# Optimization experiments

Measured on AMD Instinct MI355X. Metric: run time of the kernel, lower is better.

The kernel has to match this reference:

```python
import jax, jax.numpy as jnp
import numpy as np

N, E, DIN, H, C, ED = 50000, 500000, 264, 4, 32, 16
HID = H * C   # 128
OUT = 128
NEG_SLOPE = 0.2
LN_EPS = 1e-5


def _ln(x, g, b):
    mu = jnp.mean(x, axis=-1, keepdims=True)
    var = jnp.mean((x - mu) ** 2, axis=-1, keepdims=True)
    return (x - mu) * jax.lax.rsqrt(var + LN_EPS) * g + b


def _segment_softmax(scores, seg, num_segments):
    # scores: (E, H), seg: (E,) destination node ids
    m = jax.ops.segment_max(scores, seg, num_segments=num_segments)
    m = jnp.where(jnp.isfinite(m), m, 0.0)
    ex = jnp.exp(scores - m[seg])
    s = jax.ops.segment_sum(ex, seg, num_segments=num_segments)
    return ex / (s[seg] + 1e-16)


def _gatv2(x, src, dst, edge_attr, Wl, bl, Wr, br, We, att, bias):
    # GATv2Conv (PyG semantics): lin_l -> source, lin_r -> target, lin_edge (no bias)
    n = x.shape[0]
    xl = (x @ Wl + bl).reshape(n, H, C)          # source transform
    xr = (x @ Wr + br).reshape(n, H, C)          # target transform
    ee = (edge_attr @ We).reshape(-1, H, C)      # (E, H, C)
    m = xl[src] + xr[dst] + ee                   # per-edge pre-activation
    g = jnp.where(m > 0, m, NEG_SLOPE * m)       # leaky_relu(0.2)
    score = jnp.einsum('ehc,hc->eh', g, att)     # (E, H)
    alpha = _segment_softmax(score, dst, n)      # softmax over in-edges of each dst
    msg = xl[src] * alpha[..., None]             # (E, H, C)
    out = jax.ops.segment_sum(msg, dst, num_segments=n)
    return out.reshape(n, HID) + bias


def setup_inputs() -> dict:
    key = jax.random.key(0)
    ks = jax.random.split(key, 16)
    r = lambda k, s: jax.random.normal(k, s, dtype=jnp.float32) * 0.05
    return {
        'x': jax.random.normal(ks[0], (N, DIN), jnp.float32),
        'edge_attr': jax.random.normal(ks[1], (E, ED), jnp.float32),
        'Wl1': r(ks[2], (DIN, HID)), 'bl1': jnp.zeros((HID,), jnp.float32),
        'Wr1': r(ks[3], (DIN, HID)), 'br1': jnp.zeros((HID,), jnp.float32),
        'We1': r(ks[4], (ED, HID)), 'att1': r(ks[5], (H, C)), 'bias1': jnp.zeros((HID,), jnp.float32),
        'Wl2': r(ks[6], (HID, HID)), 'bl2': jnp.zeros((HID,), jnp.float32),
        'Wr2': r(ks[7], (HID, HID)), 'br2': jnp.zeros((HID,), jnp.float32),
        'We2': r(ks[8], (ED, HID)), 'att2': r(ks[9], (H, C)), 'bias2': jnp.zeros((HID,), jnp.float32),
        'Wres': r(ks[10], (DIN, HID)), 'bres': jnp.zeros((HID,), jnp.float32),
        'Wout': r(ks[11], (HID, OUT)), 'bout': jnp.zeros((OUT,), jnp.float32),
        'g1': jnp.ones((HID,), jnp.float32), 'bn1': jnp.zeros((HID,), jnp.float32),
        'g2': jnp.ones((HID,), jnp.float32), 'bn2': jnp.zeros((HID,), jnp.float32),
        'go': jnp.ones((OUT,), jnp.float32), 'bo': jnp.zeros((OUT,), jnp.float32),
        'edge_index': jax.random.randint(ks[12], (2, E), 0, N, dtype=jnp.int32),
    }


def reference(x, edge_attr, Wl1, bl1, Wr1, br1, We1, att1, bias1,
              Wl2, bl2, Wr2, br2, We2, att2, bias2,
              Wres, bres, Wout, bout, g1, bn1, g2, bn2, go, bo, edge_index):
    src, dst = edge_index[0], edge_index[1]
    residual = x @ Wres + bres
    h = _gatv2(x, src, dst, edge_attr, Wl1, bl1, Wr1, br1, We1, att1, bias1)
    h = jax.nn.elu(h)
    h = _ln(h + residual, g1, bn1)
    residual = h
    h = _gatv2(h, src, dst, edge_attr, Wl2, bl2, Wr2, br2, We2, att2, bias2)
    h = jax.nn.elu(h)
    h = _ln(h + residual, g2, bn2)
    context = _ln(h @ Wout + bout, go, bo)
    return context
```

## Files before the change

### kernel.cpp

```cpp
#include <hip/hip_runtime.h>
#include <hip/hip_bf16.h>
#include <math.h>
#include <stdint.h>

#define NN 50000
#define NE 500000
#define DIN 264
#define KP1 288
#define HID 128
#define EDIM 16

typedef __attribute__((ext_vector_type(8))) short short8;
typedef __attribute__((ext_vector_type(4))) float f32x4;

__device__ __forceinline__ short f2bf(float v) {
    union { float f; unsigned u; } x; x.f = v;
    unsigned r = x.u + 0x7fff + ((x.u >> 16) & 1);
    return (short)(r >> 16);
}
__device__ __forceinline__ float bf2f(short v) {
    union { float f; unsigned u; } x;
    x.u = ((unsigned)(unsigned short)v) << 16;
    return x.f;
}

__device__ __forceinline__ void gload_lds16(const void* g, void* l) {
    __builtin_amdgcn_global_load_lds(
        (const __attribute__((address_space(1))) unsigned int*)g,
        (__attribute__((address_space(3))) unsigned int*)l, 16, 0, 0);
}

__global__ void k_count(const int* __restrict__ dst, int* __restrict__ cnt) {
    int e = blockIdx.x * blockDim.x + threadIdx.x;
    if (e < NE) atomicAdd(&cnt[dst[e]], 1);
}

__global__ __launch_bounds__(256) void k_scan1(const int* __restrict__ cnt,
                                               int* __restrict__ off, int* __restrict__ bsum) {
    __shared__ int buf[256];
    int b = blockIdx.x, t = threadIdx.x;
    int i = b * 256 + t;
    int v = (i < NN) ? cnt[i] : 0;
    buf[t] = v; __syncthreads();
    for (int s = 1; s < 256; s <<= 1) {
        int u = (t >= s) ? buf[t - s] : 0; __syncthreads();
        buf[t] += u; __syncthreads();
    }
    if (i < NN) off[i + 1] = buf[t];
    if (t == 255) bsum[b] = buf[255];
}

__global__ void k_scan2(int* __restrict__ bsum, int nb) {
    __shared__ int buf[256];
    int t = threadIdx.x;
    int o = (t < nb) ? bsum[t] : 0;
    buf[t] = o; __syncthreads();
    for (int s = 1; s < 256; s <<= 1) {
        int u = (t >= s) ? buf[t - s] : 0; __syncthreads();
        buf[t] += u; __syncthreads();
    }
    if (t < nb) bsum[t] = buf[t] - o;
}

__global__ void k_scan3c(int* __restrict__ off, const int* __restrict__ bsum,
                         int* __restrict__ cur) {
    int j = blockIdx.x * 256 + threadIdx.x;
    if (j > NN) return;
    int v = (j == 0) ? 0 : off[j] + bsum[(j - 1) >> 8];
    off[j] = v;
    if (j < NN) cur[j] = v;
}

__global__ void k_scatter(const int* __restrict__ src, const int* __restrict__ dst,
                          int* __restrict__ cur, int2* __restrict__ csr_se) {
    int e = blockIdx.x * blockDim.x + threadIdx.x;
    if (e < NE) {
        int d = dst[e];
        int p = atomicAdd(&cur[d], 1);
        csr_se[p] = make_int2(src[e], e);
    }
}

__global__ void k_cvt_x(const float* __restrict__ x, short* __restrict__ xb) {
    int idx = blockIdx.x * 256 + threadIdx.x;
    if (idx >= NN * KP1) return;
    int i = idx / KP1, k = idx - i * KP1;
    xb[idx] = (k < DIN) ? f2bf(x[(size_t)i * DIN + k]) : (short)0;
}

__global__ void k_prep_w(const float* __restrict__ Wl1, const float* __restrict__ Wr1,
                         const float* __restrict__ Wres, const float* __restrict__ Wl2,
                         const float* __restrict__ Wr2, const float* __restrict__ Wout,
                         const float* __restrict__ bl1, const float* __restrict__ br1,
                         const float* __restrict__ bres, const float* __restrict__ bl2,
                         const float* __restrict__ br2,
                         short* __restrict__ Wt1, short* __restrict__ Wt2,
                         short* __restrict__ Wt3, float* __restrict__ bcat1,
                         float* __restrict__ bcat2) {
    int idx = blockIdx.x * 256 + threadIdx.x;
    if (idx < 384 * KP1) {
        int n = idx / KP1, k = idx - n * KP1;
        float v = 0.f;
        if (k < DIN) {
            const float* W = (n < 128) ? Wl1 : ((n < 256) ? Wr1 : Wres);
            v = W[(size_t)k * 128 + (n & 127)];
        }
        Wt1[idx] = f2bf(v);
        return;
    }
    idx -= 384 * KP1;
    if (idx < 256 * 128) {
        int n = idx >> 7, k = idx & 127;
        const float* W = (n < 128) ? Wl2 : Wr2;
        Wt2[idx] = f2bf(W[(size_t)k * 128 + (n & 127)]);
        return;
    }
    idx -= 256 * 128;
    if (idx < 128 * 128) {
        int n = idx >> 7, k = idx & 127;
        Wt3[idx] = f2bf(Wout[(size_t)k * 128 + n]);
        return;
    }
    idx -= 128 * 128;
    if (idx < 384) {
        bcat1[idx] = (idx < 128) ? bl1[idx] : ((idx < 256) ? br1[idx - 128] : bres[idx - 256]);
        return;
    }
    idx -= 384;
    if (idx < 256)
        bcat2[idx] = (idx < 128) ? bl2[idx] : br2[idx - 128];
}

template <bool BF16OUT>
__global__ __launch_bounds__(256) void k_mfma_gemm(const short* __restrict__ A,
                                                   const short* __restrict__ Bt,
                                                   const float* __restrict__ bias,
                                                   float* __restrict__ Cf,
                                                   short* __restrict__ Cb,
                                                   int M, int Kpad, int NS) {
    __shared__ short As[128 * 32];
    __shared__ short Bs[128 * 32];
    int t = threadIdx.x;
    int lane = t & 63, wid = t >> 6;
    int wm = (wid & 1) * 64, wn = (wid >> 1) * 64;
    int cl = lane & 15, quad = lane >> 4;
    int row0 = blockIdx.x * 128;
    int col0 = blockIdx.y * 128;

    f32x4 acc[4][4];
#pragma unroll
    for (int i = 0; i < 4; ++i)
#pragma unroll
        for (int j = 0; j < 4; ++j) acc[i][j] = (f32x4)0.f;

    for (int k0 = 0; k0 < Kpad; k0 += 32) {
#pragma unroll
        for (int r = 0; r < 2; ++r) {
            int c = t + r * 256;
            int m = c >> 2;
            int row = row0 + m; if (row >= M) row = M - 1;
            const char* ga = (const char*)A + ((size_t)row * Kpad + k0) * 2 + (c & 3) * 16;
            gload_lds16(ga, (char*)As + c * 16);
            int n = col0 + m;
            const char* gb = (const char*)Bt + ((size_t)n * Kpad + k0) * 2 + (c & 3) * 16;
            gload_lds16(gb, (char*)Bs + c * 16);
        }
        __syncthreads();

        short8 a[4], b[4];
#pragma unroll
        for (int mi = 0; mi < 4; ++mi)
            a[mi] = *(const short8*)&As[(wm + mi * 16 + cl) * 32 + quad * 8];
#pragma unroll
        for (int ni = 0; ni < 4; ++ni)
            b[ni] = *(const short8*)&Bs[(wn + ni * 16 + cl) * 32 + quad * 8];
#pragma unroll
        for (int mi = 0; mi < 4; ++mi)
#pragma unroll
            for (int ni = 0; ni < 4; ++ni)
                acc[mi][ni] = __builtin_amdgcn_mfma_f32_16x16x32_bf16(a[mi], b[ni], acc[mi][ni], 0, 0, 0);
        __syncthreads();
    }

#pragma unroll
    for (int mi = 0; mi < 4; ++mi)
#pragma unroll
        for (int ni = 0; ni < 4; ++ni) {
            int col = col0 + wn + ni * 16 + cl;
            float bv = bias[col];
#pragma unroll
            for (int r = 0; r < 4; ++r) {
                int row = row0 + wm + mi * 16 + quad * 4 + r;
                if (row < M) {
                    float v = acc[mi][ni][r] + bv;
                    if (BF16OUT) Cb[(size_t)row * NS + col] = f2bf(v);
                    else         Cf[(size_t)row * NS + col] = v;
                }
            }
        }
}

__device__ __forceinline__ float block_sum128(float v, volatile float* red) {
#pragma unroll
    for (int o = 32; o > 0; o >>= 1) v += __shfl_down(v, o, 64);
    int w = threadIdx.x >> 6;
    __syncthreads();
    if ((threadIdx.x & 63) == 0) red[w] = v;
    __syncthreads();
    return red[0] + red[1];
}

template <int STRIDE, int NPB>
__global__ __launch_bounds__(128) void k_fused_agg(const int* __restrict__ off,
                                                   const int2* __restrict__ csr_se,
                                                   const short* __restrict__ C,
                                                   const float* __restrict__ ea,
                                                   const float* __restrict__ We,
                                                   const float* __restrict__ att,
                                                   const short* __restrict__ resid, int rstride,
                                                   const float* __restrict__ bias,
                                                   const float* __restrict__ gamma,
                                                   const float* __restrict__ beta,
                                                   short* __restrict__ outb) {
    __shared__ float red[2];
    int t = threadIdx.x;

    float wreg[EDIM];
#pragma unroll
    for (int k = 0; k < EDIM; ++k) wreg[k] = We[k * 128 + t];
    float att_t = att[t], bias_t = bias[t], gamma_t = gamma[t], beta_t = beta[t];

    for (int n = 0; n < NPB; ++n) {
        int i = blockIdx.x * NPB + n;
        int b0 = off[i], b1 = off[i + 1];
        float xr_t = bf2f(C[(size_t)i * STRIDE + 128 + t]);

        float l_run = 0.f, acc = 0.f;
        int pos = b0;
        for (; pos + 2 <= b1; pos += 2) {
            int2 seA = csr_se[pos];
            int2 seB = csr_se[pos + 1];
            const float4* eaA = (const float4*)(ea + (size_t)seA.y * EDIM);
            const float4* eaB = (const float4*)(ea + (size_t)seB.y * EDIM);
            float4 A0 = eaA[0], A1 = eaA[1], A2 = eaA[2], A3 = eaA[3];
            float4 B0 = eaB[0], B1 = eaB[1], B2 = eaB[2], B3 = eaB[3];
            float xlA = bf2f(C[(size_t)seA.x * STRIDE + t]);
            float xlB = bf2f(C[(size_t)seB.x * STRIDE + t]);
            float eA = A0.x * wreg[0];
            eA = fmaf(A0.y, wreg[1], eA);  eA = fmaf(A0.z, wreg[2], eA);
            eA = fmaf(A0.w, wreg[3], eA);  eA = fmaf(A1.x, wreg[4], eA);
            eA = fmaf(A1.y, wreg[5], eA);  eA = fmaf(A1.z, wreg[6], eA);
            eA = fmaf(A1.w, wreg[7], eA);  eA = fmaf(A2.x, wreg[8], eA);
            eA = fmaf(A2.y, wreg[9], eA);  eA = fmaf(A2.z, wreg[10], eA);
            eA = fmaf(A2.w, wreg[11], eA); eA = fmaf(A3.x, wreg[12], eA);
            eA = fmaf(A3.y, wreg[13], eA); eA = fmaf(A3.z, wreg[14], eA);
            eA = fmaf(A3.w, wreg[15], eA);
            float mA = xlA + xr_t + eA;
            float pA = fmaxf(mA, 0.2f * mA) * att_t;
            float eB = B0.x * wreg[0];
            eB = fmaf(B0.y, wreg[1], eB);  eB = fmaf(B0.z, wreg[2], eB);
            eB = fmaf(B0.w, wreg[3], eB);  eB = fmaf(B1.x, wreg[4], eB);
            eB = fmaf(B1.y, wreg[5], eB);  eB = fmaf(B1.z, wreg[6], eB);
            eB = fmaf(B1.w, wreg[7], eB);  eB = fmaf(B2.x, wreg[8], eB);
            eB = fmaf(B2.y, wreg[9], eB);  eB = fmaf(B2.z, wreg[10], eB);
            eB = fmaf(B2.w, wreg[11], eB); eB = fmaf(B3.x, wreg[12], eB);
            eB = fmaf(B3.y, wreg[13], eB); eB = fmaf(B3.z, wreg[14], eB);
            eB = fmaf(B3.w, wreg[15], eB);
            float mB = xlB + xr_t + eB;
            float pB = fmaxf(mB, 0.2f * mB) * att_t;
            pA += __shfl_xor(pA, 1, 64);  pB += __shfl_xor(pB, 1, 64);
            pA += __shfl_xor(pA, 2, 64);  pB += __shfl_xor(pB, 2, 64);
            pA += __shfl_xor(pA, 4, 64);  pB += __shfl_xor(pB, 4, 64);
            pA += __shfl_xor(pA, 8, 64);  pB += __shfl_xor(pB, 8, 64);
            pA += __shfl_xor(pA, 16, 64); pB += __shfl_xor(pB, 16, 64);
            float peA = __expf(pA), peB = __expf(pB);
            l_run += peA + peB;
            acc = fmaf(peA, xlA, acc);
            acc = fmaf(peB, xlB, acc);
        }
        if (pos < b1) {
            int2 se = csr_se[pos];
            const float4* ea4 = (const float4*)(ea + (size_t)se.y * EDIM);
            float4 A0 = ea4[0], A1 = ea4[1], A2 = ea4[2], A3 = ea4[3];
            float xlv = bf2f(C[(size_t)se.x * STRIDE + t]);
            float ee = A0.x * wreg[0];
            ee = fmaf(A0.y, wreg[1], ee);  ee = fmaf(A0.z, wreg[2], ee);
            ee = fmaf(A0.w, wreg[3], ee);  ee = fmaf(A1.x, wreg[4], ee);
            ee = fmaf(A1.y, wreg[5], ee);  ee = fmaf(A1.z, wreg[6], ee);
            ee = fmaf(A1.w, wreg[7], ee);  ee = fmaf(A2.x, wreg[8], ee);
            ee = fmaf(A2.y, wreg[9], ee);  ee = fmaf(A2.z, wreg[10], ee);
            ee = fmaf(A2.w, wreg[11], ee); ee = fmaf(A3.x, wreg[12], ee);
            ee = fmaf(A3.y, wreg[13], ee); ee = fmaf(A3.z, wreg[14], ee);
            ee = fmaf(A3.w, wreg[15], ee);
            float m = xlv + xr_t + ee;
            float p = fmaxf(m, 0.2f * m) * att_t;
            p += __shfl_xor(p, 1, 64);
            p += __shfl_xor(p, 2, 64);
            p += __shfl_xor(p, 4, 64);
            p += __shfl_xor(p, 8, 64);
            p += __shfl_xor(p, 16, 64);
            float pe = __expf(p);
            l_run += pe;
            acc = fmaf(pe, xlv, acc);
        }

        float o = acc / (l_run + 1e-16f) + bias_t;
        o = o > 0.f ? o : (__expf(o) - 1.f);
        float v = o + bf2f(resid[(size_t)i * rstride + t]);
        float mean = block_sum128(v, red) * (1.f / 128.f);
        float d = v - mean;
        float var = block_sum128(d * d, red) * (1.f / 128.f);
        float r = d * rsqrtf(var + 1e-5f) * gamma_t + beta_t;
        outb[(size_t)i * 128 + t] = f2bf(r);
    }
}

__global__ __launch_bounds__(128) void k_ln(const float* __restrict__ in,
                                            const float* __restrict__ gamma,
                                            const float* __restrict__ beta,
                                            float* __restrict__ out) {
    __shared__ float red[2];
    int i = blockIdx.x, t = threadIdx.x;
    float v = in[(size_t)i * 128 + t];
    float mean = block_sum128(v, red) * (1.f / 128.f);
    float d = v - mean;
    float var = block_sum128(d * d, red) * (1.f / 128.f);
    out[(size_t)i * 128 + t] = d * rsqrtf(var + 1e-5f) * gamma[t] + beta[t];
}

extern "C" void kernel_launch(void* const* d_in, const int* in_sizes, int n_in,
                              void* d_out, int out_size, void* d_ws, size_t ws_size,
                              hipStream_t stream) {
    (void)in_sizes; (void)n_in; (void)out_size; (void)ws_size;
    const float* x     = (const float*)d_in[0];
    const float* ea    = (const float*)d_in[1];
    const float* Wl1   = (const float*)d_in[2];
    const float* bl1   = (const float*)d_in[3];
    const float* Wr1   = (const float*)d_in[4];
    const float* br1   = (const float*)d_in[5];
    const float* We1   = (const float*)d_in[6];
    const float* att1  = (const float*)d_in[7];
    const float* bias1 = (const float*)d_in[8];
    const float* Wl2   = (const float*)d_in[9];
    const float* bl2   = (const float*)d_in[10];
    const float* Wr2   = (const float*)d_in[11];
    const float* br2   = (const float*)d_in[12];
    const float* We2   = (const float*)d_in[13];
    const float* att2  = (const float*)d_in[14];
    const float* bias2 = (const float*)d_in[15];
    const float* Wres  = (const float*)d_in[16];
    const float* bres  = (const float*)d_in[17];
    const float* Wout  = (const float*)d_in[18];
    const float* bout  = (const float*)d_in[19];
    const float* g1    = (const float*)d_in[20];
    const float* bn1   = (const float*)d_in[21];
    const float* g2    = (const float*)d_in[22];
    const float* bn2   = (const float*)d_in[23];
    const float* go    = (const float*)d_in[24];
    const float* bo    = (const float*)d_in[25];
    const int*   ei    = (const int*)d_in[26];
    const int* srcv = ei;
    const int* dstv = ei + NE;
    float* outp = (float*)d_out;

    char* p = (char*)d_ws;
    auto carve = [&](size_t bytes) {
        char* r = p;
        p += (bytes + 255) & ~(size_t)255;
        return r;
    };
    short* xb    = (short*)carve((size_t)NN * KP1 * 2);
    short* Wt1   = (short*)carve((size_t)384 * KP1 * 2);
    short* Wt2   = (short*)carve((size_t)256 * 128 * 2);
    short* Wt3   = (short*)carve((size_t)128 * 128 * 2);
    float* bcat1 = (float*)carve(384 * 4);
    float* bcat2 = (float*)carve(256 * 4);
    short* C1    = (short*)carve((size_t)NN * 384 * 2);
    short* h1b   = (short*)carve((size_t)NN * 128 * 2);
    short* h2b   = (short*)carve((size_t)NN * 128 * 2);
    float* C3    = (float*)carve((size_t)NN * 128 * 4);
    int* off     = (int*)carve((size_t)(NN + 1) * 4);
    int* cur     = (int*)carve((size_t)NN * 4);
    int* bsum    = (int*)carve(256 * 4);
    int2* csr_se = (int2*)carve((size_t)NE * 8);

    short* C2 = C1;

    const int NB = (NN + 255) / 256;

    hipMemsetAsync(cur, 0, (size_t)NN * 4, stream);
    k_count<<<(NE + 255) / 256, 256, 0, stream>>>(dstv, cur);
    k_scan1<<<NB, 256, 0, stream>>>(cur, off, bsum);
    k_scan2<<<1, 256, 0, stream>>>(bsum, NB);
    k_scan3c<<<(NN + 256) / 256, 256, 0, stream>>>(off, bsum, cur);
    k_scatter<<<(NE + 255) / 256, 256, 0, stream>>>(srcv, dstv, cur, csr_se);

    k_cvt_x<<<((size_t)NN * KP1 + 255) / 256, 256, 0, stream>>>(x, xb);
    int prep_total = 384 * KP1 + 256 * 128 + 128 * 128 + 384 + 256;
    k_prep_w<<<(prep_total + 255) / 256, 256, 0, stream>>>(Wl1, Wr1, Wres, Wl2, Wr2, Wout,
                                                           bl1, br1, bres, bl2, br2,
                                                           Wt1, Wt2, Wt3, bcat1, bcat2);

    int mb = (NN + 127) / 128;

    k_mfma_gemm<true><<<dim3(mb, 3), 256, 0, stream>>>(xb, Wt1, bcat1, nullptr, C1, NN, KP1, 384);
    k_fused_agg<384, 4><<<NN / 4, 128, 0, stream>>>(off, csr_se, C1, ea, We1, att1,
                                                    C1 + 256, 384, bias1, g1, bn1, h1b);
    k_mfma_gemm<true><<<dim3(mb, 2), 256, 0, stream>>>(h1b, Wt2, bcat2, nullptr, C2, NN, 128, 256);
    k_fused_agg<256, 4><<<NN / 4, 128, 0, stream>>>(off, csr_se, C2, ea, We2, att2,
                                                    h1b, 128, bias2, g2, bn2, h2b);
    k_mfma_gemm<false><<<dim3(mb, 1), 256, 0, stream>>>(h2b, Wt3, bout, C3, nullptr, NN, 128, 128);
    k_ln<<<NN, 128, 0, stream>>>(C3, go, bo, outp);
}
```

Baseline: 528.8 us.

## Fuse final GEMM with LayerNorm and map one wavefront per node in aggregation

```diff
diff --git a/kernel.cpp b/kernel.cpp
--- a/kernel.cpp
+++ b/kernel.cpp
@@ -22,6 +22,12 @@
     union { float f; unsigned u; } x;
     x.u = ((unsigned)(unsigned short)v) << 16;
     return x.f;
+}
+__device__ __forceinline__ float bflo(unsigned u) {
+    union { float f; unsigned u; } x; x.u = u << 16; return x.f;
+}
+__device__ __forceinline__ float bfhi(unsigned u) {
+    union { float f; unsigned u; } x; x.u = u & 0xffff0000u; return x.f;
 }
 
 __device__ __forceinline__ void gload_lds16(const void* g, void* l) {
@@ -200,18 +206,161 @@
         }
 }
 
-__device__ __forceinline__ float block_sum128(float v, volatile float* red) {
-#pragma unroll
-    for (int o = 32; o > 0; o >>= 1) v += __shfl_down(v, o, 64);
-    int w = threadIdx.x >> 6;
+__global__ __launch_bounds__(256) void k_gemm_ln(const short* __restrict__ A,
+                                                 const short* __restrict__ Bt,
+                                                 const float* __restrict__ bias,
+                                                 const float* __restrict__ gamma,
+                                                 const float* __restrict__ beta,
+                                                 float* __restrict__ out, int M) {
+    __shared__ short As[128 * 32];
+    __shared__ short Bs[128 * 32];
+    __shared__ float redS[128][2];
+    int t = threadIdx.x;
+    int lane = t & 63, wid = t >> 6;
+    int wm = (wid & 1) * 64, wn = (wid >> 1) * 64;
+    int cl = lane & 15, quad = lane >> 4;
+    int row0 = blockIdx.x * 128;
+    int wh = wid >> 1;
+
+    f32x4 acc[4][4];
+#pragma unroll
+    for (int i = 0; i < 4; ++i)
+#pragma unroll
+        for (int j = 0; j < 4; ++j) acc[i][j] = (f32x4)0.f;
+
+    for (int k0 = 0; k0 < 128; k0 += 32) {
+#pragma unroll
+        for (int r = 0; r < 2; ++r) {
+            int c = t + r * 256;
+            int m = c >> 2;
+            int row = row0 + m; if (row >= M) row = M - 1;
+            const char* ga = (const char*)A + ((size_t)row * 128 + k0) * 2 + (c & 3) * 16;
+            gload_lds16(ga, (char*)As + c * 16);
+            const char* gb = (const char*)Bt + ((size_t)m * 128 + k0) * 2 + (c & 3) * 16;
+            gload_lds16(gb, (char*)Bs + c * 16);
+        }
+        __syncthreads();
+
+        short8 a[4], b[4];
+#pragma unroll
+        for (int mi = 0; mi < 4; ++mi)
+            a[mi] = *(const short8*)&As[(wm + mi * 16 + cl) * 32 + quad * 8];
+#pragma unroll
+        for (int ni = 0; ni < 4; ++ni)
+            b[ni] = *(const short8*)&Bs[(wn + ni * 16 + cl) * 32 + quad * 8];
+#pragma unroll
+        for (int mi = 0; mi < 4; ++mi)
+#pragma unroll
+            for (int ni = 0; ni < 4; ++ni)
+                acc[mi][ni] = __builtin_amdgcn_mfma_f32_16x16x32_bf16(a[mi], b[ni], acc[mi][ni], 0, 0, 0);
+        __syncthreads();
+    }
+
+    float bv[4], gv[4], bev[4];
+#pragma unroll
+    for (int ni = 0; ni < 4; ++ni) {
+        int col = wn + ni * 16 + cl;
+        bv[ni] = bias[col]; gv[ni] = gamma[col]; bev[ni] = beta[col];
+    }
+
+    float s[4][4];
+#pragma unroll
+    for (int mi = 0; mi < 4; ++mi)
+#pragma unroll
+        for (int r = 0; r < 4; ++r) {
+            float v = (acc[mi][0][r] + bv[0]) + (acc[mi][1][r] + bv[1]) +
+                      (acc[mi][2][r] + bv[2]) + (acc[mi][3][r] + bv[3]);
+            v += __shfl_xor(v, 1, 64);
+            v += __shfl_xor(v, 2, 64);
+            v += __shfl_xor(v, 4, 64);
+            v += __shfl_xor(v, 8, 64);
+            s[mi][r] = v;
+        }
+    if (cl == 0) {
+#pragma unroll
+        for (int mi = 0; mi < 4; ++mi)
+#pragma unroll
+            for (int r = 0; r < 4; ++r)
+                redS[wm + mi * 16 + quad * 4 + r][wh] = s[mi][r];
+    }
     __syncthreads();
-    if ((threadIdx.x & 63) == 0) red[w] = v;
+    float mean[4][4];
+#pragma unroll
+    for (int mi = 0; mi < 4; ++mi)
+#pragma unroll
+        for (int r = 0; r < 4; ++r) {
+            int rl = wm + mi * 16 + quad * 4 + r;
+            mean[mi][r] = (redS[rl][0] + redS[rl][1]) * (1.f / 128.f);
+        }
     __syncthreads();
-    return red[0] + red[1];
-}
-
-template <int STRIDE, int NPB>
-__global__ __launch_bounds__(128) void k_fused_agg(const int* __restrict__ off,
+
+#pragma unroll
+    for (int mi = 0; mi < 4; ++mi)
+#pragma unroll
+        for (int r = 0; r < 4; ++r) {
+            float q = 0.f;
+#pragma unroll
+            for (int ni = 0; ni < 4; ++ni) {
+                float d = acc[mi][ni][r] + bv[ni] - mean[mi][r];
+                q = fmaf(d, d, q);
+            }
+            q += __shfl_xor(q, 1, 64);
+            q += __shfl_xor(q, 2, 64);
+            q += __shfl_xor(q, 4, 64);
+            q += __shfl_xor(q, 8, 64);
+            s[mi][r] = q;
+        }
+    if (cl == 0) {
+#pragma unroll
+        for (int mi = 0; mi < 4; ++mi)
+#pragma unroll
+            for (int r = 0; r < 4; ++r)
+                redS[wm + mi * 16 + quad * 4 + r][wh] = s[mi][r];
+    }
+    __syncthreads();
+
+#pragma unroll
+    for (int mi = 0; mi < 4; ++mi)
+#pragma unroll
+        for (int r = 0; r < 4; ++r) {
+            int rl = wm + mi * 16 + quad * 4 + r;
+            int row = row0 + rl;
+            if (row < M) {
+                float rstd = rsqrtf((redS[rl][0] + redS[rl][1]) * (1.f / 128.f) + 1e-5f);
+#pragma unroll
+                for (int ni = 0; ni < 4; ++ni) {
+                    int col = wn + ni * 16 + cl;
+                    float d = acc[mi][ni][r] + bv[ni] - mean[mi][r];
+                    out[(size_t)row * 128 + col] = fmaf(d * rstd, gv[ni], bev[ni]);
+                }
+            }
+        }
+}
+
+__device__ __forceinline__ void edot16(const float4 E0, const float4 E1,
+                                       const float4 E2, const float4 E3,
+                                       const float2* __restrict__ w,
+                                       float& o0, float& o1) {
+    o0 = E0.x * w[0].x;            o1 = E0.x * w[0].y;
+    o0 = fmaf(E0.y, w[1].x, o0);   o1 = fmaf(E0.y, w[1].y, o1);
+    o0 = fmaf(E0.z, w[2].x, o0);   o1 = fmaf(E0.z, w[2].y, o1);
+    o0 = fmaf(E0.w, w[3].x, o0);   o1 = fmaf(E0.w, w[3].y, o1);
+    o0 = fmaf(E1.x, w[4].x, o0);   o1 = fmaf(E1.x, w[4].y, o1);
+    o0 = fmaf(E1.y, w[5].x, o0);   o1 = fmaf(E1.y, w[5].y, o1);
+    o0 = fmaf(E1.z, w[6].x, o0);   o1 = fmaf(E1.z, w[6].y, o1);
+    o0 = fmaf(E1.w, w[7].x, o0);   o1 = fmaf(E1.w, w[7].y, o1);
+    o0 = fmaf(E2.x, w[8].x, o0);   o1 = fmaf(E2.x, w[8].y, o1);
+    o0 = fmaf(E2.y, w[9].x, o0);   o1 = fmaf(E2.y, w[9].y, o1);
+    o0 = fmaf(E2.z, w[10].x, o0);  o1 = fmaf(E2.z, w[10].y, o1);
+    o0 = fmaf(E2.w, w[11].x, o0);  o1 = fmaf(E2.w, w[11].y, o1);
+    o0 = fmaf(E3.x, w[12].x, o0);  o1 = fmaf(E3.x, w[12].y, o1);
+    o0 = fmaf(E3.y, w[13].x, o0);  o1 = fmaf(E3.y, w[13].y, o1);
+    o0 = fmaf(E3.z, w[14].x, o0);  o1 = fmaf(E3.z, w[14].y, o1);
+    o0 = fmaf(E3.w, w[15].x, o0);  o1 = fmaf(E3.w, w[15].y, o1);
+}
+
+template <int STRIDE>
+__global__ __launch_bounds__(256) void k_fused_agg(const int* __restrict__ off,
                                                    const int2* __restrict__ csr_se,
                                                    const short* __restrict__ C,
                                                    const float* __restrict__ ea,
@@ -222,110 +371,95 @@
                                                    const float* __restrict__ gamma,
                                                    const float* __restrict__ beta,
                                                    short* __restrict__ outb) {
-    __shared__ float red[2];
     int t = threadIdx.x;
-
-    float wreg[EDIM];
-#pragma unroll
-    for (int k = 0; k < EDIM; ++k) wreg[k] = We[k * 128 + t];
-    float att_t = att[t], bias_t = bias[t], gamma_t = gamma[t], beta_t = beta[t];
-
-    for (int n = 0; n < NPB; ++n) {
-        int i = blockIdx.x * NPB + n;
-        int b0 = off[i], b1 = off[i + 1];
-        float xr_t = bf2f(C[(size_t)i * STRIDE + 128 + t]);
-
-        float l_run = 0.f, acc = 0.f;
-        int pos = b0;
-        for (; pos + 2 <= b1; pos += 2) {
-            int2 seA = csr_se[pos];
-            int2 seB = csr_se[pos + 1];
-            const float4* eaA = (const float4*)(ea + (size_t)seA.y * EDIM);
-            const float4* eaB = (const float4*)(ea + (size_t)seB.y * EDIM);
-            float4 A0 = eaA[0], A1 = eaA[1], A2 = eaA[2], A3 = eaA[3];
-            float4 B0 = eaB[0], B1 = eaB[1], B2 = eaB[2], B3 = eaB[3];
-            float xlA = bf2f(C[(size_t)seA.x * STRIDE + t]);
-            float xlB = bf2f(C[(size_t)seB.x * STRIDE + t]);
-            float eA = A0.x * wreg[0];
-            eA = fmaf(A0.y, wreg[1], eA);  eA = fmaf(A0.z, wreg[2], eA);
-            eA = fmaf(A0.w, wreg[3], eA);  eA = fmaf(A1.x, wreg[4], eA);
-            eA = fmaf(A1.y, wreg[5], eA);  eA = fmaf(A1.z, wreg[6], eA);
-            eA = fmaf(A1.w, wreg[7], eA);  eA = fmaf(A2.x, wreg[8], eA);
-            eA = fmaf(A2.y, wreg[9], eA);  eA = fmaf(A2.z, wreg[10], eA);
-            eA = fmaf(A2.w, wreg[11], eA); eA = fmaf(A3.x, wreg[12], eA);
-            eA = fmaf(A3.y, wreg[13], eA); eA = fmaf(A3.z, wreg[14], eA);
-            eA = fmaf(A3.w, wreg[15], eA);
-            float mA = xlA + xr_t + eA;
-            float pA = fmaxf(mA, 0.2f * mA) * att_t;
-            float eB = B0.x * wreg[0];
-            eB = fmaf(B0.y, wreg[1], eB);  eB = fmaf(B0.z, wreg[2], eB);
-            eB = fmaf(B0.w, wreg[3], eB);  eB = fmaf(B1.x, wreg[4], eB);
-            eB = fmaf(B1.y, wreg[5], eB);  eB = fmaf(B1.z, wreg[6], eB);
-            eB = fmaf(B1.w, wreg[7], eB);  eB = fmaf(B2.x, wreg[8], eB);
-            eB = fmaf(B2.y, wreg[9], eB);  eB = fmaf(B2.z, wreg[10], eB);
-            eB = fmaf(B2.w, wreg[11], eB); eB = fmaf(B3.x, wreg[12], eB);
-            eB = fmaf(B3.y, wreg[13], eB); eB = fmaf(B3.z, wreg[14], eB);
-            eB = fmaf(B3.w, wreg[15], eB);
-            float mB = xlB + xr_t + eB;
-            float pB = fmaxf(mB, 0.2f * mB) * att_t;
-            pA += __shfl_xor(pA, 1, 64);  pB += __shfl_xor(pB, 1, 64);
-            pA += __shfl_xor(pA, 2, 64);  pB += __shfl_xor(pB, 2, 64);
-            pA += __shfl_xor(pA, 4, 64);  pB += __shfl_xor(pB, 4, 64);
-            pA += __shfl_xor(pA, 8, 64);  pB += __shfl_xor(pB, 8, 64);
-            pA += __shfl_xor(pA, 16, 64); pB += __shfl_xor(pB, 16, 64);
-            float peA = __expf(pA), peB = __expf(pB);
-            l_run += peA + peB;
-            acc = fmaf(peA, xlA, acc);
-            acc = fmaf(peB, xlB, acc);
-        }
-        if (pos < b1) {
-            int2 se = csr_se[pos];
-            const float4* ea4 = (const float4*)(ea + (size_t)se.y * EDIM);
-            float4 A0 = ea4[0], A1 = ea4[1], A2 = ea4[2], A3 = ea4[3];
-            float xlv = bf2f(C[(size_t)se.x * STRIDE + t]);
-            float ee = A0.x * wreg[0];
-            ee = fmaf(A0.y, wreg[1], ee);  ee = fmaf(A0.z, wreg[2], ee);
-            ee = fmaf(A0.w, wreg[3], ee);  ee = fmaf(A1.x, wreg[4], ee);
-            ee = fmaf(A1.y, wreg[5], ee);  ee = fmaf(A1.z, wreg[6], ee);
-            ee = fmaf(A1.w, wreg[7], ee);  ee = fmaf(A2.x, wreg[8], ee);
-            ee = fmaf(A2.y, wreg[9], ee);  ee = fmaf(A2.z, wreg[10], ee);
-            ee = fmaf(A2.w, wreg[11], ee); ee = fmaf(A3.x, wreg[12], ee);
-            ee = fmaf(A3.y, wreg[13], ee); ee = fmaf(A3.z, wreg[14], ee);
-            ee = fmaf(A3.w, wreg[15], ee);
-            float m = xlv + xr_t + ee;
-            float p = fmaxf(m, 0.2f * m) * att_t;
-            p += __shfl_xor(p, 1, 64);
-            p += __shfl_xor(p, 2, 64);
-            p += __shfl_xor(p, 4, 64);
-            p += __shfl_xor(p, 8, 64);
-            p += __shfl_xor(p, 16, 64);
-            float pe = __expf(p);
-            l_run += pe;
-            acc = fmaf(pe, xlv, acc);
-        }
-
-        float o = acc / (l_run + 1e-16f) + bias_t;
-        o = o > 0.f ? o : (__expf(o) - 1.f);
-        float v = o + bf2f(resid[(size_t)i * rstride + t]);
-        float mean = block_sum128(v, red) * (1.f / 128.f);
-        float d = v - mean;
-        float var = block_sum128(d * d, red) * (1.f / 128.f);
-        float r = d * rsqrtf(var + 1e-5f) * gamma_t + beta_t;
-        outb[(size_t)i * 128 + t] = f2bf(r);
-    }
-}
-
-__global__ __launch_bounds__(128) void k_ln(const float* __restrict__ in,
-                                            const float* __restrict__ gamma,
-                                            const float* __restrict__ beta,
-                                            float* __restrict__ out) {
-    __shared__ float red[2];
-    int i = blockIdx.x, t = threadIdx.x;
-    float v = in[(size_t)i * 128 + t];
-    float mean = block_sum128(v, red) * (1.f / 128.f);
-    float d = v - mean;
-    float var = block_sum128(d * d, red) * (1.f / 128.f);
-    out[(size_t)i * 128 + t] = d * rsqrtf(var + 1e-5f) * gamma[t] + beta[t];
+    int w = t >> 6, l = t & 63;
+    int f0 = (l >> 4) * 32 + (l & 15) * 2;
+    int fp = f0 >> 1;
+
+    float2 wreg[16];
+    const float2* We2 = (const float2*)We;
+#pragma unroll
+    for (int k = 0; k < 16; ++k) wreg[k] = We2[k * 64 + fp];
+    float2 av = ((const float2*)att)[fp];
+    float2 bs2 = ((const float2*)bias)[fp];
+    float2 gv = ((const float2*)gamma)[fp];
+    float2 bev = ((const float2*)beta)[fp];
+
+    int i = blockIdx.x * 4 + w;
+    unsigned xrp = *(const unsigned*)&C[(size_t)i * STRIDE + 128 + f0];
+    float xr0 = bflo(xrp), xr1 = bfhi(xrp);
+
+    int b0 = off[i], b1 = off[i + 1];
+    float l_run = 0.f, acc0 = 0.f, acc1 = 0.f;
+    int pos = b0;
+    for (; pos + 2 <= b1; pos += 2) {
+        int2 seA = csr_se[pos];
+        int2 seB = csr_se[pos + 1];
+        const float4* eaA = (const float4*)(ea + (size_t)seA.y * EDIM);
+        const float4* eaB = (const float4*)(ea + (size_t)seB.y * EDIM);
+        float4 A0 = eaA[0], A1 = eaA[1], A2 = eaA[2], A3 = eaA[3];
+        float4 B0 = eaB[0], B1 = eaB[1], B2 = eaB[2], B3 = eaB[3];
+        unsigned xlA = *(const unsigned*)&C[(size_t)seA.x * STRIDE + f0];
+        unsigned xlB = *(const unsigned*)&C[(size_t)seB.x * STRIDE + f0];
+        float eA0, eA1, eB0, eB1;
+        edot16(A0, A1, A2, A3, wreg, eA0, eA1);
+        edot16(B0, B1, B2, B3, wreg, eB0, eB1);
+        float xa0 = bflo(xlA), xa1 = bfhi(xlA);
+        float xb0 = bflo(xlB), xb1 = bfhi(xlB);
+        float mA0 = xa0 + xr0 + eA0, mA1 = xa1 + xr1 + eA1;
+        float mB0 = xb0 + xr0 + eB0, mB1 = xb1 + xr1 + eB1;
+        float pA = fmaf(fmaxf(mA1, 0.2f * mA1), av.y, fmaxf(mA0, 0.2f * mA0) * av.x);
+        float pB = fmaf(fmaxf(mB1, 0.2f * mB1), av.y, fmaxf(mB0, 0.2f * mB0) * av.x);
+        pA += __shfl_xor(pA, 1, 64);  pB += __shfl_xor(pB, 1, 64);
+        pA += __shfl_xor(pA, 2, 64);  pB += __shfl_xor(pB, 2, 64);
+        pA += __shfl_xor(pA, 4, 64);  pB += __shfl_xor(pB, 4, 64);
+        pA += __shfl_xor(pA, 8, 64);  pB += __shfl_xor(pB, 8, 64);
+        float peA = __expf(pA), peB = __expf(pB);
+        l_run += peA + peB;
+        acc0 = fmaf(peA, xa0, acc0); acc1 = fmaf(peA, xa1, acc1);
+        acc0 = fmaf(peB, xb0, acc0); acc1 = fmaf(peB, xb1, acc1);
+    }
+    if (pos < b1) {
+        int2 se = csr_se[pos];
+        const float4* ea4 = (const float4*)(ea + (size_t)se.y * EDIM);
+        float4 A0 = ea4[0], A1 = ea4[1], A2 = ea4[2], A3 = ea4[3];
+        unsigned xlv = *(const unsigned*)&C[(size_t)se.x * STRIDE + f0];
+        float e0, e1;
+        edot16(A0, A1, A2, A3, wreg, e0, e1);
+        float x0 = bflo(xlv), x1 = bfhi(xlv);
+        float m0 = x0 + xr0 + e0, m1 = x1 + xr1 + e1;
+        float p = fmaf(fmaxf(m1, 0.2f * m1), av.y, fmaxf(m0, 0.2f * m0) * av.x);
+        p += __shfl_xor(p, 1, 64);
+        p += __shfl_xor(p, 2, 64);
+        p += __shfl_xor(p, 4, 64);
+        p += __shfl_xor(p, 8, 64);
+        float pe = __expf(p);
+        l_run += pe;
+        acc0 = fmaf(pe, x0, acc0);
+        acc1 = fmaf(pe, x1, acc1);
+    }
+
+    float inv = 1.f / (l_run + 1e-16f);
+    float o0 = fmaf(acc0, inv, bs2.x);
+    float o1 = fmaf(acc1, inv, bs2.y);
+    o0 = o0 > 0.f ? o0 : (__expf(o0) - 1.f);
+    o1 = o1 > 0.f ? o1 : (__expf(o1) - 1.f);
+    unsigned rp = *(const unsigned*)&resid[(size_t)i * rstride + f0];
+    float v0 = o0 + bflo(rp), v1 = o1 + bfhi(rp);
+    float s = v0 + v1;
+#pragma unroll
+    for (int o = 32; o > 0; o >>= 1) s += __shfl_xor(s, o, 64);
+    float mean = s * (1.f / 128.f);
+    float d0 = v0 - mean, d1 = v1 - mean;
+    float q = fmaf(d0, d0, d1 * d1);
+#pragma unroll
+    for (int o = 32; o > 0; o >>= 1) q += __shfl_xor(q, o, 64);
+    float rstd = rsqrtf(q * (1.f / 128.f) + 1e-5f);
+    float r0 = fmaf(d0 * rstd, gv.x, bev.x);
+    float r1 = fmaf(d1 * rstd, gv.y, bev.y);
+    unsigned op = (unsigned)(unsigned short)f2bf(r0) |
+                  (((unsigned)(unsigned short)f2bf(r1)) << 16);
+    *(unsigned*)&outb[(size_t)i * 128 + f0] = op;
 }
 
 extern "C" void kernel_launch(void* const* d_in, const int* in_sizes, int n_in,
@@ -378,7 +512,6 @@
     short* C1    = (short*)carve((size_t)NN * 384 * 2);
     short* h1b   = (short*)carve((size_t)NN * 128 * 2);
     short* h2b   = (short*)carve((size_t)NN * 128 * 2);
-    float* C3    = (float*)carve((size_t)NN * 128 * 4);
     int* off     = (int*)carve((size_t)(NN + 1) * 4);
     int* cur     = (int*)carve((size_t)NN * 4);
     int* bsum    = (int*)carve(256 * 4);
@@ -404,11 +537,10 @@
     int mb = (NN + 127) / 128;
 
     k_mfma_gemm<true><<<dim3(mb, 3), 256, 0, stream>>>(xb, Wt1, bcat1, nullptr, C1, NN, KP1, 384);
-    k_fused_agg<384, 4><<<NN / 4, 128, 0, stream>>>(off, csr_se, C1, ea, We1, att1,
-                                                    C1 + 256, 384, bias1, g1, bn1, h1b);
+    k_fused_agg<384><<<NN / 4, 256, 0, stream>>>(off, csr_se, C1, ea, We1, att1,
+                                                 C1 + 256, 384, bias1, g1, bn1, h1b);
     k_mfma_gemm<true><<<dim3(mb, 2), 256, 0, stream>>>(h1b, Wt2, bcat2, nullptr, C2, NN, 128, 256);
-    k_fused_agg<256, 4><<<NN / 4, 128, 0, stream>>>(off, csr_se, C2, ea, We2, att2,
-                                                    h1b, 128, bias2, g2, bn2, h2b);
-    k_mfma_gemm<false><<<dim3(mb, 1), 256, 0, stream>>>(h2b, Wt3, bout, C3, nullptr, NN, 128, 128);
-    k_ln<<<NN, 128, 0, stream>>>(C3, go, bo, outp);
-}
+    k_fused_agg<256><<<NN / 4, 256, 0, stream>>>(off, csr_se, C2, ea, We2, att2,
+                                                 h1b, 128, bias2, g2, bn2, h2b);
+    k_gemm_ln<<<mb, 256, 0, stream>>>(h2b, Wt3, bout, go, bo, outp, NN);
+}
```

New measurement: 564.9 us. 6.8% more time.
